# Kernel tuning notes

Measured on AMD Instinct MI355X. Metric: run time of the kernel, lower is better.

The kernel has to match this reference:

```python
import jax, jax.numpy as jnp
import numpy as np

N, CIN, T, V = 64, 192, 256, 25
K, COUT, S = 3, 64, 5  # kernel_size, out_channels, num_semantic


def setup_inputs() -> dict:
    key = jax.random.key(0)
    ks = jax.random.split(key, 8)
    x = jax.random.normal(ks[0], (N, CIN, T, V), jnp.float32)
    A = jax.random.normal(ks[1], (K, V, V), jnp.float32)
    node_type = jnp.arange(V, dtype=jnp.int64) % S  # every semantic type present
    Wc = jax.random.normal(ks[2], (COUT * K, CIN), jnp.float32) * 0.02
    bc = jax.random.normal(ks[3], (COUT * K,), jnp.float32) * 0.02
    W1 = jax.random.normal(ks[4], (S * COUT, COUT * K), jnp.float32) * 0.02
    b1 = jax.random.normal(ks[5], (S * COUT,), jnp.float32) * 0.02
    W2 = jax.random.normal(ks[6], (S * COUT, COUT * K), jnp.float32) * 0.02
    b2 = jax.random.normal(ks[7], (S * COUT,), jnp.float32) * 0.02
    return {"x": x, "A": A, "node_type": node_type, "Wc": Wc, "bc": bc,
            "W1": W1, "b1": b1, "W2": W2, "b2": b2}


def reference(x, A, node_type, Wc, bc, W1, b1, W2, b2):
    # self.conv: 1x1 conv (t_kernel_size=1) -> (N, K*COUT, T, V)
    y = jnp.einsum('nctv,oc->notv', x, Wc) + bc[None, :, None, None]
    # conv1 / conv2 applied to tmp_x = y, reshape to (N, S, COUT, T, V), mean over T
    x1 = (jnp.einsum('nctv,oc->notv', y, W1) + b1[None, :, None, None]).reshape(N, S, COUT, T, V)
    x2 = (jnp.einsum('nctv,oc->notv', y, W2) + b2[None, :, None, None]).reshape(N, S, COUT, T, V)
    x1 = x1.mean(axis=3, keepdims=True)  # (N, S, COUT, 1, V)
    x2 = x2.mean(axis=3, keepdims=True)  # (N, S, COUT, 1, V)
    # per-semantic masked mean over nodes (vectorized over the 5 semantic types)
    masks = (node_type[None, :] == jnp.arange(S)[:, None]).astype(y.dtype)  # (S, V)
    counts = masks.sum(axis=-1)  # (S,)
    sem = jnp.einsum('nsclv,sv->nscl', x1, masks) / counts[None, :, None, None]  # (N,S,COUT,1)
    # diff: (N, S, COUT, 1, 1, V)  (graph_list stacked over the semantic axis)
    graphs = sem[..., None, None] - x2[:, :, :, :, None, :]
    # graph conv with adjacency A
    xk = y.reshape(N, K, COUT, T, V)
    out = jnp.einsum('nkctv,kvw->nctw', xk, A)  # (N, COUT, T, V)
    return out, A, graphs
```

## Files before the change

### kernel.cpp

```cpp
#include <hip/hip_runtime.h>

#define N_    64
#define CIN_  192
#define T_    256
#define V_    25
#define K_    3
#define COUT_ 64
#define OC_   192
#define SS_   5

#define OUT_OFF_A (N_*COUT_*T_*V_)
#define OUT_OFF_G (OUT_OFF_A + K_*V_*V_)

#define TCH   2
#define HCH   16
#define NCOLS 50
#define NCT   4
#define XB_STRIDE 200
#define XB_ROWS 64
#define XB_SH  (XB_ROWS*XB_STRIDE)
#define YB_STRIDE 104
#define YB_ROWS 128
#define YB_OFF  XB_SH
#define U_SHORTS (YB_OFF + YB_ROWS*YB_STRIDE)
#define NYV  4800
#define CPN  (T_/(TCH*HCH))
#define NBLK (N_*CPN)
#define SUNITS (25*(CIN_/8))
#define UPT 3

#define BAR_LDS() do {                                          \
    __builtin_amdgcn_sched_barrier(0);                          \
    asm volatile("s_waitcnt lgkmcnt(0)" ::: "memory");          \
    __builtin_amdgcn_s_barrier();                               \
    __builtin_amdgcn_sched_barrier(0);                          \
} while (0)

typedef __attribute__((ext_vector_type(8))) short short8;
typedef __attribute__((ext_vector_type(4))) float float4v;

__device__ inline unsigned bf16r(float f) {
    unsigned u = __float_as_uint(f);
    return (u + 0x7fffu + ((u >> 16) & 1u)) >> 16;
}

__global__ __launch_bounds__(256) void prep(const float* __restrict__ Wc,
                                            const float* __restrict__ A,
                                            short* __restrict__ WcB,
                                            short* __restrict__ A2T,
                                            float* __restrict__ ysum,
                                            float* __restrict__ out) {
    int idx = blockIdx.x * 256 + threadIdx.x;
    if (idx < OC_ * CIN_) WcB[idx] = (short)bf16r(Wc[idx]);
    if (idx < 32 * YB_STRIDE) {
        int w = idx / YB_STRIDE, kk = idx - w * YB_STRIDE;
        short val = 0;
        if (w < V_ && kk < K_ * V_) {
            int k = kk / V_, v = kk - k * V_;
            val = (short)bf16r(A[k * V_ * V_ + v * V_ + w]);
        }
        A2T[idx] = val;
    }
    if (idx < K_ * V_ * V_) out[OUT_OFF_A + idx] = A[idx];
    if (idx < N_ * NYV) ysum[idx] = 0.f;
}

__global__ __launch_bounds__(256, 2) void fused_mfma(const float* __restrict__ x,
                                                     const short* __restrict__ WcB,
                                                     const float* __restrict__ bc,
                                                     const short* __restrict__ A2T,
                                                     float* __restrict__ out,
                                                     float* __restrict__ ysum) {
    __shared__ __align__(16) short U[U_SHORTS];
    __shared__ __align__(16) short A2l[32 * YB_STRIDE];

    const int tid  = threadIdx.x;
    const int lane = tid & 63;
    const int wv   = tid >> 6;
    const int l15  = lane & 15;
    const int q    = lane >> 4;
    const int n    = blockIdx.x >> 3;
    const int tc   = blockIdx.x & 7;
    const int rt0  = wv * 3;

    {
        int4 z = make_int4(0, 0, 0, 0);
        for (int i = tid; i < U_SHORTS / 8; i += 256) ((int4*)U)[i] = z;
        for (int i = tid; i < 32 * YB_STRIDE / 2; i += 256)
            ((int*)A2l)[i] = ((const int*)A2T)[i];
    }
    __syncthreads();

    short8 wfrag[3][6];
    {
        const short* wb = WcB + (rt0 * 16 + l15) * CIN_ + q * 8;
#pragma unroll
        for (int j = 0; j < 3; ++j)
#pragma unroll
            for (int ks = 0; ks < 6; ++ks)
                wfrag[j][ks] = *(const short8*)(wb + j * 16 * CIN_ + ks * 32);
    }
    float4v bvec[3];
#pragma unroll
    for (int j = 0; j < 3; ++j)
        bvec[j] = *(const float4v*)(bc + (rt0 + j) * 16 + q * 4);

    float racc[19];
#pragma unroll
    for (int u = 0; u < 19; ++u) racc[u] = 0.f;

    const float* xn = x + (size_t)n * (CIN_ * T_ * V_);
    const int tbase = tc * (TCH * HCH);

    for (int u = tid; u < SUNITS; u += 256) {
        int col2 = u % 25, cg = u / 25;
        const float* xp = xn + (size_t)(cg * 8) * (T_ * V_) + tbase * V_ + col2 * 2;
        short8 a, b;
#pragma unroll
        for (int j = 0; j < 8; ++j) {
            float2 f = *(const float2*)(xp + (size_t)j * (T_ * V_));
            a[j] = (short)bf16r(f.x);
            b[j] = (short)bf16r(f.y);
        }
        *(short8*)&U[(col2 * 2 + 0) * XB_STRIDE + cg * 8] = a;
        *(short8*)&U[(col2 * 2 + 1) * XB_STRIDE + cg * 8] = b;
    }

    for (int h = 0; h < HCH; ++h) {
        const int t0 = tbase + h * TCH;
        const bool stage_ok = (h < HCH - 1);

        BAR_LDS();

        float2 tmp[UPT][8];
        if (stage_ok) {
#pragma unroll
            for (int s = 0; s < UPT; ++s) {
                int u = tid + s * 256;
                if (u < SUNITS) {
                    int col2 = u % 25, cg = u / 25;
                    const float* xp = xn + (size_t)(cg * 8) * (T_ * V_) + (t0 + TCH) * V_ + col2 * 2;
#pragma unroll
                    for (int j = 0; j < 8; ++j)
                        tmp[s][j] = *(const float2*)(xp + (size_t)j * (T_ * V_));
                }
            }
            __builtin_amdgcn_sched_barrier(0);
        }

        float4v acc[3][NCT];
#pragma unroll
        for (int j = 0; j < 3; ++j)
#pragma unroll
            for (int ct = 0; ct < NCT; ++ct) acc[j][ct] = bvec[j];

#pragma unroll
        for (int ct = 0; ct < NCT; ++ct) {
            const short* xb = &U[(ct * 16 + l15) * XB_STRIDE + q * 8];
#pragma unroll
            for (int ks = 0; ks < 6; ++ks) {
                short8 bfrag = *(const short8*)(xb + ks * 32);
#pragma unroll
                for (int j = 0; j < 3; ++j)
                    acc[j][ct] = __builtin_amdgcn_mfma_f32_16x16x32_bf16(
                        wfrag[j][ks], bfrag, acc[j][ct], 0, 0, 0);
            }
        }

#pragma unroll
        for (int ct = 0; ct < NCT; ++ct) {
            int col = ct * 16 + l15;
            if (col < NCOLS) {
                int tl = col / V_;
                int v  = col - tl * V_;
#pragma unroll
                for (int j = 0; j < 3; ++j) {
                    int obase = (rt0 + j) * 16 + q * 4;
#pragma unroll
                    for (int i = 0; i < 4; ++i) {
                        int o   = obase + i;
                        int row = tl * 64 + (o & 63);
                        int cY  = (o >> 6) * V_ + v;
                        U[YB_OFF + row * YB_STRIDE + cY] = (short)bf16r(acc[j][ct][i]);
                    }
                }
            }
        }

        BAR_LDS();

        short8 b2[2][3];
#pragma unroll
        for (int nt = 0; nt < 2; ++nt)
#pragma unroll
            for (int ks = 0; ks < 3; ++ks)
                b2[nt][ks] = *(const short8*)&A2l[(nt * 16 + l15) * YB_STRIDE + ks * 32 + q * 8];

        float4v o2[2][2];
#pragma unroll
        for (int mt = 0; mt < 2; ++mt)
#pragma unroll
            for (int nt = 0; nt < 2; ++nt) o2[mt][nt] = (float4v){0.f, 0.f, 0.f, 0.f};

#pragma unroll
        for (int mt = 0; mt < 2; ++mt) {
            int m = (wv * 2 + mt) * 16 + l15;
            const short* yb = &U[YB_OFF + m * YB_STRIDE + q * 8];
#pragma unroll
            for (int ks = 0; ks < 3; ++ks) {
                short8 af = *(const short8*)(yb + ks * 32);
#pragma unroll
                for (int nt = 0; nt < 2; ++nt)
                    o2[mt][nt] = __builtin_amdgcn_mfma_f32_16x16x32_bf16(
                        af, b2[nt][ks], o2[mt][nt], 0, 0, 0);
            }
        }

#pragma unroll
        for (int mt = 0; mt < 2; ++mt) {
#pragma unroll
            for (int nt = 0; nt < 2; ++nt) {
                int w = nt * 16 + l15;
                if (w < V_) {
#pragma unroll
                    for (int i = 0; i < 4; ++i) {
                        int m  = (wv * 2 + mt) * 16 + q * 4 + i;
                        int cc = m & 63, tl = m >> 6;
                        out[((size_t)(n * COUT_ + cc) * T_ + (t0 + tl)) * V_ + w] = o2[mt][nt][i];
                    }
                }
            }
        }

#pragma unroll
        for (int u = 0; u < 19; ++u) {
            int idx = tid + u * 256;
            if (u < 18 || idx < NYV) {
                int o = idx / V_, v = idx - (idx / V_) * V_;
                int cc = o & 63, k = o >> 6;
                const short* yp = &U[YB_OFF + cc * YB_STRIDE + k * V_ + v];
                float s = 0.f;
#pragma unroll
                for (int tl = 0; tl < TCH; ++tl) {
                    unsigned b = (unsigned short)yp[tl * 64 * YB_STRIDE];
                    s += __uint_as_float(b << 16);
                }
                racc[u] += s;
            }
        }

        if (stage_ok) {
#pragma unroll
            for (int s = 0; s < UPT; ++s) {
                int u = tid + s * 256;
                if (u < SUNITS) {
                    int col2 = u % 25, cg = u / 25;
                    short8 a, b;
#pragma unroll
                    for (int j = 0; j < 8; ++j) {
                        a[j] = (short)bf16r(tmp[s][j].x);
                        b[j] = (short)bf16r(tmp[s][j].y);
                    }
                    *(short8*)&U[(col2 * 2 + 0) * XB_STRIDE + cg * 8] = a;
                    *(short8*)&U[(col2 * 2 + 1) * XB_STRIDE + cg * 8] = b;
                }
            }
        }
    }

    float* yb = ysum + (size_t)n * NYV;
#pragma unroll
    for (int u = 0; u < 19; ++u) {
        int idx = tid + u * 256;
        if (u < 18 || idx < NYV) atomicAdd(&yb[idx], racc[u]);
    }
}

__global__ __launch_bounds__(256) void e2_graphs(const float* __restrict__ ysum,
                                                 const float* __restrict__ W1,
                                                 const float* __restrict__ b1,
                                                 const float* __restrict__ W2,
                                                 const float* __restrict__ b2,
                                                 const int* __restrict__ node_type,
                                                 float* __restrict__ out) {
    __shared__ float s1[10][V_];
    __shared__ float sem[10];
    const int tid = threadIdx.x;
    const int n  = blockIdx.x >> 5;
    const int jc = blockIdx.x & 31;
    const int jl = tid / V_;
    const int v  = tid - jl * V_;
    const int j  = jc * 10 + jl;
    float x2 = 0.f;
    if (jl < 10) {
        const float* yb = ysum + (size_t)n * NYV + v;
        const float* w1 = W1 + j * OC_;
        const float* w2 = W2 + j * OC_;
        float a1 = 0.f, a2 = 0.f;
        for (int o = 0; o < OC_; ++o) {
            float yv = yb[o * V_];
            a1 += w1[o] * yv;
            a2 += w2[o] * yv;
        }
        s1[jl][v] = b1[j] + a1 * (1.0f / T_);
        x2 = b2[j] + a2 * (1.0f / T_);
    }
    __syncthreads();
    if (tid < 10) {
        int s = (jc * 10 + tid) >> 6;
        float sum = 0.f, cnt = 0.f;
        for (int vv = 0; vv < V_; ++vv)
            if (node_type[vv] == s) { sum += s1[tid][vv]; cnt += 1.f; }
        sem[tid] = sum / cnt;
    }
    __syncthreads();
    if (jl < 10)
        out[OUT_OFF_G + (size_t)n * (SS_ * COUT_ * V_) + j * V_ + v] = sem[jl] - x2;
}

extern "C" void kernel_launch(void* const* d_in, const int* in_sizes, int n_in,
                              void* d_out, int out_size, void* d_ws, size_t ws_size,
                              hipStream_t stream) {
    const float* x         = (const float*)d_in[0];
    const float* A         = (const float*)d_in[1];
    const int*   node_type = (const int*)d_in[2];
    const float* Wc        = (const float*)d_in[3];
    const float* bc        = (const float*)d_in[4];
    const float* W1        = (const float*)d_in[5];
    const float* b1        = (const float*)d_in[6];
    const float* W2        = (const float*)d_in[7];
    const float* b2        = (const float*)d_in[8];
    float* out = (float*)d_out;

    float* ysum = (float*)d_ws;
    short* WcB  = (short*)(ysum + N_ * NYV);
    short* A2T  = WcB + OC_ * CIN_;

    hipLaunchKernelGGL(prep, dim3((N_ * NYV + 255) / 256), dim3(256), 0, stream,
                       Wc, A, WcB, A2T, ysum, out);
    hipLaunchKernelGGL(fused_mfma, dim3(NBLK), dim3(256), 0, stream,
                       x, WcB, bc, A2T, out, ysum);
    hipLaunchKernelGGL(e2_graphs, dim3(N_ * 32), dim3(256), 0, stream,
                       ysum, W1, b1, W2, b2, node_type, out);
}
```

Before: 566.7 us.

## Swap MFMA operands and permute columns so Y stores pack two bf16s

The first GEMM now swaps its A/B operands so each lane holds a fixed output channel across four columns. The x staging columns are permuted so (tl=0,tl=1) pairs for the same node land in adjacent accumulator slots. The Y buffer is re-laid out with k stride 32, which lets the epilogue write packed 32-bit pairs instead of 12 scattered 16-bit LDS stores per tile. The A2T layout and the y-sum reads are updated to match. This cuts LDS store instructions and address arithmetic, at the cost of more complex index mapping that must stay consistent across the prep kernel and the consumers.

```diff
diff --git a/kernel.cpp b/kernel.cpp
--- a/kernel.cpp
+++ b/kernel.cpp
@@ -44,6 +44,10 @@
     return (u + 0x7fffu + ((u >> 16) & 1u)) >> 16;
 }
 
+__device__ inline int ncol(int f) {
+    return (f < 25) ? f * 2 : (f - 25) * 2 + 1;
+}
+
 __global__ __launch_bounds__(256) void prep(const float* __restrict__ Wc,
                                             const float* __restrict__ A,
                                             short* __restrict__ WcB,
@@ -55,9 +59,9 @@
     if (idx < 32 * YB_STRIDE) {
         int w = idx / YB_STRIDE, kk = idx - w * YB_STRIDE;
         short val = 0;
-        if (w < V_ && kk < K_ * V_) {
-            int k = kk / V_, v = kk - k * V_;
-            val = (short)bf16r(A[k * V_ * V_ + v * V_ + w]);
+        if (w < V_ && kk < 96) {
+            int k = kk >> 5, v = kk & 31;
+            if (v < V_) val = (short)bf16r(A[k * V_ * V_ + v * V_ + w]);
         }
         A2T[idx] = val;
     }
@@ -100,10 +104,9 @@
             for (int ks = 0; ks < 6; ++ks)
                 wfrag[j][ks] = *(const short8*)(wb + j * 16 * CIN_ + ks * 32);
     }
-    float4v bvec[3];
-#pragma unroll
-    for (int j = 0; j < 3; ++j)
-        bvec[j] = *(const float4v*)(bc + (rt0 + j) * 16 + q * 4);
+    float bcs[3];
+#pragma unroll
+    for (int j = 0; j < 3; ++j) bcs[j] = bc[(rt0 + j) * 16 + l15];
 
     float racc[19];
 #pragma unroll
@@ -113,8 +116,8 @@
     const int tbase = tc * (TCH * HCH);
 
     for (int u = tid; u < SUNITS; u += 256) {
-        int col2 = u % 25, cg = u / 25;
-        const float* xp = xn + (size_t)(cg * 8) * (T_ * V_) + tbase * V_ + col2 * 2;
+        int f0 = (u % 25) * 2, cg = u / 25;
+        const float* xp = xn + (size_t)(cg * 8) * (T_ * V_) + tbase * V_ + f0;
         short8 a, b;
 #pragma unroll
         for (int j = 0; j < 8; ++j) {
@@ -122,8 +125,8 @@
             a[j] = (short)bf16r(f.x);
             b[j] = (short)bf16r(f.y);
         }
-        *(short8*)&U[(col2 * 2 + 0) * XB_STRIDE + cg * 8] = a;
-        *(short8*)&U[(col2 * 2 + 1) * XB_STRIDE + cg * 8] = b;
+        *(short8*)&U[ncol(f0) * XB_STRIDE + cg * 8] = a;
+        *(short8*)&U[ncol(f0 + 1) * XB_STRIDE + cg * 8] = b;
     }
 
     for (int h = 0; h < HCH; ++h) {
@@ -138,8 +141,8 @@
             for (int s = 0; s < UPT; ++s) {
                 int u = tid + s * 256;
                 if (u < SUNITS) {
-                    int col2 = u % 25, cg = u / 25;
-                    const float* xp = xn + (size_t)(cg * 8) * (T_ * V_) + (t0 + TCH) * V_ + col2 * 2;
+                    int f0 = (u % 25) * 2, cg = u / 25;
+                    const float* xp = xn + (size_t)(cg * 8) * (T_ * V_) + (t0 + TCH) * V_ + f0;
 #pragma unroll
                     for (int j = 0; j < 8; ++j)
                         tmp[s][j] = *(const float2*)(xp + (size_t)j * (T_ * V_));
@@ -152,7 +155,8 @@
 #pragma unroll
         for (int j = 0; j < 3; ++j)
 #pragma unroll
-            for (int ct = 0; ct < NCT; ++ct) acc[j][ct] = bvec[j];
+            for (int ct = 0; ct < NCT; ++ct)
+                acc[j][ct] = (float4v){bcs[j], bcs[j], bcs[j], bcs[j]};
 
 #pragma unroll
         for (int ct = 0; ct < NCT; ++ct) {
@@ -163,26 +167,28 @@
 #pragma unroll
                 for (int j = 0; j < 3; ++j)
                     acc[j][ct] = __builtin_amdgcn_mfma_f32_16x16x32_bf16(
-                        wfrag[j][ks], bfrag, acc[j][ct], 0, 0, 0);
-            }
-        }
-
-#pragma unroll
-        for (int ct = 0; ct < NCT; ++ct) {
-            int col = ct * 16 + l15;
-            if (col < NCOLS) {
-                int tl = col / V_;
-                int v  = col - tl * V_;
-#pragma unroll
-                for (int j = 0; j < 3; ++j) {
-                    int obase = (rt0 + j) * 16 + q * 4;
-#pragma unroll
-                    for (int i = 0; i < 4; ++i) {
-                        int o   = obase + i;
-                        int row = tl * 64 + (o & 63);
-                        int cY  = (o >> 6) * V_ + v;
-                        U[YB_OFF + row * YB_STRIDE + cY] = (short)bf16r(acc[j][ct][i]);
-                    }
+                        bfrag, wfrag[j][ks], acc[j][ct], 0, 0, 0);
+            }
+        }
+
+#pragma unroll
+        for (int j = 0; j < 3; ++j) {
+            int o  = (rt0 + j) * 16 + l15;
+            int cc = o & 63, k = o >> 6;
+            int r0 = YB_OFF + cc * YB_STRIDE + k * 32;
+            int r1 = r0 + 64 * YB_STRIDE;
+#pragma unroll
+            for (int ct = 0; ct < NCT; ++ct) {
+                int colbase = ct * 16 + q * 4;
+                int v0 = colbase >> 1;
+                if (colbase <= 44) {
+                    unsigned p0 = bf16r(acc[j][ct][0]) | (bf16r(acc[j][ct][2]) << 16);
+                    unsigned p1 = bf16r(acc[j][ct][1]) | (bf16r(acc[j][ct][3]) << 16);
+                    *(unsigned*)&U[r0 + v0] = p0;
+                    *(unsigned*)&U[r1 + v0] = p1;
+                } else if (colbase == 48) {
+                    U[r0 + 24] = (short)bf16r(acc[j][ct][0]);
+                    U[r1 + 24] = (short)bf16r(acc[j][ct][1]);
                 }
             }
         }
@@ -238,7 +244,7 @@
             if (u < 18 || idx < NYV) {
                 int o = idx / V_, v = idx - (idx / V_) * V_;
                 int cc = o & 63, k = o >> 6;
-                const short* yp = &U[YB_OFF + cc * YB_STRIDE + k * V_ + v];
+                const short* yp = &U[YB_OFF + cc * YB_STRIDE + k * 32 + v];
                 float s = 0.f;
 #pragma unroll
                 for (int tl = 0; tl < TCH; ++tl) {
@@ -254,15 +260,15 @@
             for (int s = 0; s < UPT; ++s) {
                 int u = tid + s * 256;
                 if (u < SUNITS) {
-                    int col2 = u % 25, cg = u / 25;
+                    int f0 = (u % 25) * 2, cg = u / 25;
                     short8 a, b;
 #pragma unroll
                     for (int j = 0; j < 8; ++j) {
                         a[j] = (short)bf16r(tmp[s][j].x);
                         b[j] = (short)bf16r(tmp[s][j].y);
                     }
-                    *(short8*)&U[(col2 * 2 + 0) * XB_STRIDE + cg * 8] = a;
-                    *(short8*)&U[(col2 * 2 + 1) * XB_STRIDE + cg * 8] = b;
+                    *(short8*)&U[ncol(f0) * XB_STRIDE + cg * 8] = a;
+                    *(short8*)&U[ncol(f0 + 1) * XB_STRIDE + cg * 8] = b;
                 }
             }
         }
```

Result: no change. 555.8 us (median of 2 runs) (-1.9%).
